# Optimization experiments

Measured on AMD Instinct MI355X. Metric: run time of the kernel, lower is better.

Reference implementation:

```python
import jax, jax.numpy as jnp
from jax import lax
import numpy as np

NUM_SUBCNNS = 3      # num_classes - 1
C_FEAT = 1024        # backbone feature channels (hard-coded in CAM loop)
STRIDE = 32          # 224 -> 7 spatial reduction, like densenet121 features


def setup_inputs() -> dict:
    key = jax.random.key(0)
    ks = jax.random.split(key, 8)
    B, H, W = 32, 224, 224
    x = jax.random.normal(ks[0], (B, 3, H, W), dtype=jnp.float32)
    # Stand-in backbone per branch: conv 3->1024, kernel=stride=32 (same output
    # shape/dataflow as densenet121 features: [B,1024,7,7]).
    Wb = jax.random.normal(ks[1], (NUM_SUBCNNS, C_FEAT, 3, STRIDE, STRIDE), dtype=jnp.float32) * 0.02
    bb = jnp.zeros((NUM_SUBCNNS, C_FEAT), dtype=jnp.float32)
    # projection head: Linear(1024,512) -> ReLU -> (Dropout, eval=identity) -> Linear(512,2)
    p1_w = jax.random.normal(ks[2], (NUM_SUBCNNS, 512, C_FEAT), dtype=jnp.float32) * 0.02
    p1_b = jnp.zeros((NUM_SUBCNNS, 512), dtype=jnp.float32)
    p2_w = jax.random.normal(ks[3], (NUM_SUBCNNS, 2, 512), dtype=jnp.float32) * 0.02
    p2_b = jnp.zeros((NUM_SUBCNNS, 2), dtype=jnp.float32)
    # classifier Linear(1024,2): only its weight is used, for the CAM reduction
    cls_w = jax.random.normal(ks[4], (NUM_SUBCNNS, 2, C_FEAT), dtype=jnp.float32) * 0.02
    return {"x": x, "Wb": Wb, "bb": bb, "p1_w": p1_w, "p1_b": p1_b,
            "p2_w": p2_w, "p2_b": p2_b, "cls_w": cls_w}


def reference(x, Wb, bb, p1_w, p1_b, p2_w, p2_b, cls_w):
    ranking_outputs = []
    cam_outputs = []
    features_list = []
    for i in range(NUM_SUBCNNS):
        # backbone feature extraction: [B,3,224,224] -> [B,1024,7,7]
        feats = lax.conv_general_dilated(
            x, Wb[i], window_strides=(STRIDE, STRIDE), padding="VALID",
            dimension_numbers=("NCHW", "OIHW", "NCHW")) + bb[i][None, :, None, None]
        features_list.append(feats)
        # global average pool over H,W
        pooled = jnp.mean(feats, axis=(2, 3))                       # [B,1024]
        # projection MLP (dropout is identity at inference)
        h = jax.nn.relu(pooled @ p1_w[i].T + p1_b[i])               # [B,512]
        logits = h @ p2_w[i].T + p2_b[i]                            # [B,2]
        ranking_outputs.append(jax.nn.softmax(logits, axis=1)[:, 1:2])  # [B,1]
        # CAM: the torch double python-loop == one contraction over channels
        cam = jax.nn.relu(jnp.einsum("oc,bchw->obhw", cls_w[i], feats))  # [2,B,7,7]
        cam_outputs.append((cam[0], cam[1]))
    ranking = jnp.concatenate(ranking_outputs, axis=1)              # [B,3]
    return ranking, cam_outputs, features_list
```

## Files before the change

### kernel.cpp

```cpp
#include <hip/hip_runtime.h>
#include <hip/hip_bf16.h>
#include <math.h>

#define NSUB   3
#define CFEAT  1024
#define KDIM   3072
#define MDIM   1568
#define BATCH  32
#define NMT    25
#define NKT    96

#define OUT_CAM   96
#define OUT_FEAT  9504
#define FEAT_PER_BRANCH (BATCH * CFEAT * 49)

#define WS_A      0
#define WS_W      (9600 * 1024)
#define WS_POOLED (WS_W + 18432 * 1024)
#define WS_H      (WS_POOLED + NSUB * BATCH * CFEAT * 4)
#define WS_CAMP   (WS_H + NSUB * BATCH * 512 * 4)

typedef __attribute__((ext_vector_type(8))) short bf16x8;
typedef __attribute__((ext_vector_type(4))) float f32x4;

__device__ __forceinline__ short b16(float f){
    __hip_bfloat16 h = __float2bfloat16(f);
    return *reinterpret_cast<short*>(&h);
}
__device__ __forceinline__ bf16x8 pack8(float4 a, float4 b){
    bf16x8 r;
    r[0]=b16(a.x); r[1]=b16(a.y); r[2]=b16(a.z); r[3]=b16(a.w);
    r[4]=b16(b.x); r[5]=b16(b.y); r[6]=b16(b.z); r[7]=b16(b.w);
    return r;
}

__global__ __launch_bounds__(256) void prep_frag(
    const float* __restrict__ x, const float* __restrict__ w,
    bf16x8* __restrict__ Af, bf16x8* __restrict__ Wf)
{
    int bid = blockIdx.x, t = threadIdx.x;
    if (bid < 4608) {
        int g = bid * 256 + t;
        int chunk = g >> 6, l = g & 63;
        int ni = chunk & 3, KT = (chunk >> 2) % 96, NTg = chunk / 384;
        int n = NTg * 64 + ni * 16 + (l & 15);
        int k = KT * 32 + (l >> 4) * 8;
        const float* src = w + (size_t)n * KDIM + k;
        Wf[(size_t)chunk * 64 + l] = pack8(*(const float4*)src, *(const float4*)(src + 4));
    } else {
        int g = (bid - 4608) * 256 + t;
        int chunk = g >> 6, l = g & 63;
        int mi = chunk & 3, KT = (chunk >> 2) % 96, MT = chunk / 384;
        int m  = MT * 64 + mi * 16 + (l & 15);
        int k0 = KT * 32 + (l >> 4) * 8;
        bf16x8 v;
        if (m < MDIM) {
            int b = m / 49, p = m % 49, ph = p / 7, pw = p % 7;
            int ch = k0 >> 10, r = (k0 >> 5) & 31, s = k0 & 31;
            const float* src = x + (((size_t)(b*3 + ch)*224 + ph*32 + r)*224 + pw*32 + s);
            v = pack8(*(const float4*)src, *(const float4*)(src + 4));
        } else {
            v = (bf16x8){0,0,0,0,0,0,0,0};
        }
        Af[(size_t)chunk * 64 + l] = v;
    }
}

__global__ __launch_bounds__(128, 2) void conv_mfma(
    const bf16x8* __restrict__ Af, const bf16x8* __restrict__ Wf,
    const float* __restrict__ bb, float* __restrict__ out)
{
    __shared__ float eplds[2][64 * 65];

    int bid = (int)blockIdx.x;
    bid = (bid & 7) * 75 + (bid >> 3);
    const int i   = bid / 200;
    const int rem = bid % 200;
    const int NTb = rem / 25, MT = rem % 25;

    const int wv = threadIdx.x >> 6, l = threadIdx.x & 63;
    const int NT = NTb + wv * 8;
    const int lrow = l & 15, q = l >> 4;

    const bf16x8* Ab = Af + (size_t)(MT * 384) * 64 + l;
    const bf16x8* Bb = Wf + (size_t)((i*16 + NT) * 384) * 64 + l;

    f32x4 acc[4][4] = {};
    bf16x8 a0[4], b0[4], a1[4], b1[4], a2[4], b2[4];

    auto LOADT = [&](bf16x8 (&Ad)[4], bf16x8 (&Bd)[4], int KT){
        const bf16x8* An = Ab + KT * 256;
        const bf16x8* Bn = Bb + KT * 256;
#pragma unroll
        for (int m2 = 0; m2 < 4; ++m2) { Ad[m2] = An[m2*64]; Bd[m2] = Bn[m2*64]; }
    };
    auto MFMAT = [&](bf16x8 (&As)[4], bf16x8 (&Bs)[4]){
#pragma unroll
        for (int mi = 0; mi < 4; ++mi)
#pragma unroll
            for (int ni = 0; ni < 4; ++ni)
                acc[mi][ni] = __builtin_amdgcn_mfma_f32_16x16x32_bf16(
                    As[mi], Bs[ni], acc[mi][ni], 0, 0, 0);
    };

    LOADT(a0, b0, 0);
    LOADT(a1, b1, 1);
    for (int kt = 0; kt < NKT; kt += 3) {
        LOADT(a2, b2, kt + 2);
        MFMAT(a0, b0);
        if (kt + 3 < NKT) LOADT(a0, b0, kt + 3);
        MFMAT(a1, b1);
        if (kt + 4 < NKT) LOADT(a1, b1, kt + 4);
        MFMAT(a2, b2);
    }

    float bias[4];
#pragma unroll
    for (int ni = 0; ni < 4; ++ni)
        bias[ni] = bb[i*CFEAT + NT*64 + ni*16 + lrow];
    float* ep = eplds[wv];
#pragma unroll
    for (int mi = 0; mi < 4; ++mi)
#pragma unroll
        for (int ni = 0; ni < 4; ++ni)
#pragma unroll
            for (int rr = 0; rr < 4; ++rr)
                ep[(mi*16 + q*4 + rr) * 65 + ni*16 + lrow] = acc[mi][ni][rr] + bias[ni];

    float* featb = out + OUT_FEAT + (size_t)i * FEAT_PER_BRANCH;
    int m = MT*64 + l;
    if (m < MDIM) {
        int b = m / 49, p = m % 49;
        float* base = featb + (size_t)(b*CFEAT + NT*64) * 49 + p;
#pragma unroll 8
        for (int c = 0; c < 64; ++c)
            base[c * 49] = ep[l*65 + c];
    }
}

__global__ __launch_bounds__(128) void cam_pool(
    const float* __restrict__ feat, const float* __restrict__ cls_w,
    float* __restrict__ pooled, float* __restrict__ camp)
{
    __shared__ float fs[128][50];
    int bid = blockIdx.x;
    int i = bid >> 8, b = (bid >> 3) & 31, ch = bid & 7;
    int t = threadIdx.x;
    int c0 = ch * 128;
    const float* f = feat + ((size_t)(i*BATCH + b) * CFEAT + c0) * 49;

    for (int qq = 0; qq < 49; ++qq) {
        int e = qq*128 + t;
        fs[e / 49][e % 49] = f[e];
    }
    __syncthreads();

    {
        float s = 0.f;
#pragma unroll
        for (int k = 0; k < 49; ++k) s += fs[t][k];
        pooled[(size_t)(i*BATCH + b) * CFEAT + c0 + t] = s * (1.f/49.f);
    }

    if (t < 98) {
        int o = t / 49, p = t % 49;
        const float* w = cls_w + (size_t)i * 2 * CFEAT + o * CFEAT + c0;
        float s = 0.f;
        for (int c = 0; c < 128; ++c) s += w[c] * fs[c][p];
        camp[(size_t)bid * 98 + t] = s;
    }
}

__global__ __launch_bounds__(256) void mlp1_kernel(
    const float* __restrict__ pooled, const float* __restrict__ p1w,
    const float* __restrict__ p1b, float* __restrict__ h,
    const float* __restrict__ camp, float* __restrict__ out_cam)
{
    if (blockIdx.x >= 48) {
        int fid = (blockIdx.x - 48) * 256 + threadIdx.x;
        if (fid < NSUB * 2 * MDIM) {
            int io = fid / MDIM, rem = fid % MDIM;
            int b = rem / 49, p = rem % 49;
            int i = io >> 1, o = io & 1;
            float s = 0.f;
#pragma unroll
            for (int c = 0; c < 8; ++c)
                s += camp[(size_t)(((i*BATCH + b)*8) + c) * 98 + o*49 + p];
            out_cam[fid] = fmaxf(s, 0.f);
        }
        return;
    }
    __shared__ float ps[32 * 256];
    int i = blockIdx.x >> 4, jc = blockIdx.x & 15;
    int t = threadIdx.x;
    int j = jc*32 + (t & 31);
    int bg = (t >> 5) * 4;
    float acc[4] = {};
    const float* wrow = p1w + ((size_t)i*512 + j) * CFEAT;
    for (int kc = 0; kc < 4; ++kc) {
        __syncthreads();
#pragma unroll
        for (int qq = 0; qq < 8; ++qq) {
            int f4 = t + qq*256;
            int b = f4 >> 6, k4 = (f4 & 63) * 4;
            *(float4*)&ps[b*256 + k4] =
                *(const float4*)&pooled[((size_t)i*32 + b)*CFEAT + kc*256 + k4];
        }
        __syncthreads();
        const float* wk = wrow + kc*256;
        for (int k = 0; k < 256; k += 4) {
            float4 w4 = *(const float4*)(wk + k);
#pragma unroll
            for (int qq = 0; qq < 4; ++qq) {
                const float* pr = &ps[(bg + qq)*256 + k];
                acc[qq] += w4.x*pr[0] + w4.y*pr[1] + w4.z*pr[2] + w4.w*pr[3];
            }
        }
    }
    float bias = p1b[i*512 + j];
#pragma unroll
    for (int qq = 0; qq < 4; ++qq)
        h[((size_t)i*32 + bg + qq)*512 + j] = fmaxf(acc[qq] + bias, 0.f);
}

__global__ void mlp2_kernel(const float* __restrict__ h, const float* __restrict__ p2w,
                            const float* __restrict__ p2b, float* __restrict__ out)
{
    __shared__ float part[256];
    int i = blockIdx.x, t = threadIdx.x;
    int b = t & 31, kc = t >> 5;
    const float* hv = h + ((size_t)i*32 + b)*512 + kc*64;
    const float* w0 = p2w + (size_t)i*1024 + kc*64;
    const float* w1 = w0 + 512;
    float s = 0.f;
    for (int k = 0; k < 64; ++k) s += hv[k] * (w1[k] - w0[k]);
    part[t] = s;
    __syncthreads();
    if (t < 32) {
        float d = 0.f;
#pragma unroll
        for (int qq = 0; qq < 8; ++qq) d += part[qq*32 + t];
        d += p2b[i*2 + 1] - p2b[i*2 + 0];
        out[b*NSUB + i] = 1.f / (1.f + expf(-d));
    }
}

extern "C" void kernel_launch(void* const* d_in, const int* in_sizes, int n_in,
                              void* d_out, int out_size, void* d_ws, size_t ws_size,
                              hipStream_t stream)
{
    const float* x    = (const float*)d_in[0];
    const float* Wb   = (const float*)d_in[1];
    const float* bbp  = (const float*)d_in[2];
    const float* p1w  = (const float*)d_in[3];
    const float* p1b  = (const float*)d_in[4];
    const float* p2w  = (const float*)d_in[5];
    const float* p2b  = (const float*)d_in[6];
    const float* clsw = (const float*)d_in[7];
    float* out = (float*)d_out;

    char* ws = (char*)d_ws;
    bf16x8* Af    = (bf16x8*)(ws + WS_A);
    bf16x8* Wf    = (bf16x8*)(ws + WS_W);
    float* pooled = (float*)(ws + WS_POOLED);
    float* hbuf   = (float*)(ws + WS_H);
    float* camp   = (float*)(ws + WS_CAMP);

    prep_frag<<<4608 + 2400, 256, 0, stream>>>(x, Wb, Af, Wf);
    conv_mfma<<<600, 128, 0, stream>>>(Af, Wf, bbp, out);
    cam_pool<<<NSUB*BATCH*8, 128, 0, stream>>>(out + OUT_FEAT, clsw, pooled, camp);
    mlp1_kernel<<<48 + 37, 256, 0, stream>>>(pooled, p1w, p1b, hbuf, camp, out + OUT_CAM);
    mlp2_kernel<<<NSUB, 256, 0, stream>>>(hbuf, p2w, p2b, out);
}
```

Measured before the change: 109.6 us.

## Deepen GEMM register prefetch to four stages with explicit vmcnt waits

Replaces the three-buffer register pipeline in the backbone GEMM with a four-stage one. Global loads are issued through inline asm and waited on with explicit s_waitcnt vmcnt counts plus scheduling barriers, so more loads stay in flight while MFMAs run. The MFMA blocks are also wrapped in s_setprio to raise wave priority during compute. This adds 16 more VGPRs per thread for the extra buffers, which may lower occupancy, and the hand-written wait counts must match the exact number of outstanding loads.

```diff
diff --git a/kernel.cpp b/kernel.cpp
--- a/kernel.cpp
+++ b/kernel.cpp
@@ -7,7 +7,6 @@
 #define KDIM   3072
 #define MDIM   1568
 #define BATCH  32
-#define NMT    25
 #define NKT    96
 
 #define OUT_CAM   96
@@ -31,6 +30,13 @@
     bf16x8 r;
     r[0]=b16(a.x); r[1]=b16(a.y); r[2]=b16(a.z); r[3]=b16(a.w);
     r[4]=b16(b.x); r[5]=b16(b.y); r[6]=b16(b.z); r[7]=b16(b.w);
+    return r;
+}
+
+__device__ __forceinline__ bf16x8 gld16(const bf16x8* p){
+    bf16x8 r;
+    asm volatile("global_load_dwordx4 %0, %1, off"
+                 : "=v"(r) : "v"(p) : "memory");
     return r;
 }
 
@@ -86,33 +92,43 @@
     const bf16x8* Bb = Wf + (size_t)((i*16 + NT) * 384) * 64 + l;
 
     f32x4 acc[4][4] = {};
-    bf16x8 a0[4], b0[4], a1[4], b1[4], a2[4], b2[4];
-
-    auto LOADT = [&](bf16x8 (&Ad)[4], bf16x8 (&Bd)[4], int KT){
-        const bf16x8* An = Ab + KT * 256;
-        const bf16x8* Bn = Bb + KT * 256;
-#pragma unroll
-        for (int m2 = 0; m2 < 4; ++m2) { Ad[m2] = An[m2*64]; Bd[m2] = Bn[m2*64]; }
-    };
-    auto MFMAT = [&](bf16x8 (&As)[4], bf16x8 (&Bs)[4]){
-#pragma unroll
-        for (int mi = 0; mi < 4; ++mi)
-#pragma unroll
-            for (int ni = 0; ni < 4; ++ni)
-                acc[mi][ni] = __builtin_amdgcn_mfma_f32_16x16x32_bf16(
-                    As[mi], Bs[ni], acc[mi][ni], 0, 0, 0);
-    };
-
-    LOADT(a0, b0, 0);
-    LOADT(a1, b1, 1);
-    for (int kt = 0; kt < NKT; kt += 3) {
-        LOADT(a2, b2, kt + 2);
-        MFMAT(a0, b0);
-        if (kt + 3 < NKT) LOADT(a0, b0, kt + 3);
-        MFMAT(a1, b1);
-        if (kt + 4 < NKT) LOADT(a1, b1, kt + 4);
-        MFMAT(a2, b2);
-    }
+    bf16x8 a0[4], b0[4], a1[4], b1[4], a2[4], b2[4], a3[4], b3[4];
+
+#define ISSUE(Ax, Bx, KT) {                                        \
+    const bf16x8* pA_ = Ab + (KT) * 256;                           \
+    const bf16x8* pB_ = Bb + (KT) * 256;                           \
+    Ax[0] = gld16(pA_);       Ax[1] = gld16(pA_ + 64);             \
+    Ax[2] = gld16(pA_ + 128); Ax[3] = gld16(pA_ + 192);            \
+    Bx[0] = gld16(pB_);       Bx[1] = gld16(pB_ + 64);             \
+    Bx[2] = gld16(pB_ + 128); Bx[3] = gld16(pB_ + 192); }
+
+#define MFMAT(Ax, Bx) {                                            \
+    __builtin_amdgcn_s_setprio(1);                                 \
+    _Pragma("unroll") for (int mi = 0; mi < 4; ++mi)               \
+    _Pragma("unroll") for (int ni = 0; ni < 4; ++ni)               \
+        acc[mi][ni] = __builtin_amdgcn_mfma_f32_16x16x32_bf16(     \
+            Ax[mi], Bx[ni], acc[mi][ni], 0, 0, 0);                 \
+    __builtin_amdgcn_s_setprio(0); }
+
+#define WAITV(N) { asm volatile("s_waitcnt vmcnt(" #N ")" ::: "memory"); \
+                   __builtin_amdgcn_sched_barrier(0); }
+
+    ISSUE(a0, b0, 0); ISSUE(a1, b1, 1); ISSUE(a2, b2, 2); ISSUE(a3, b3, 3);
+
+    for (int kt = 0; kt <= 88; kt += 4) {
+        WAITV(24); MFMAT(a0, b0); ISSUE(a0, b0, kt + 4);
+        WAITV(24); MFMAT(a1, b1); ISSUE(a1, b1, kt + 5);
+        WAITV(24); MFMAT(a2, b2); ISSUE(a2, b2, kt + 6);
+        WAITV(24); MFMAT(a3, b3); ISSUE(a3, b3, kt + 7);
+    }
+    WAITV(24); MFMAT(a0, b0);
+    WAITV(16); MFMAT(a1, b1);
+    WAITV(8);  MFMAT(a2, b2);
+    WAITV(0);  MFMAT(a3, b3);
+
+#undef ISSUE
+#undef MFMAT
+#undef WAITV
 
     float bias[4];
 #pragma unroll
```

Result: no change. 110.4 us (+0.7%).
